# Optimization experiments

Hardware: AMD Instinct MI355X
Metric: run time of the kernel (lower is better)

## Reference

```python
import jax, jax.numpy as jnp
import numpy as np

B, O, GRID = 2048, 48, 112
SIGMA = 5.0


def setup_inputs() -> dict:
    key = jax.random.key(0)
    k1, k2, k3, k4, k5 = jax.random.split(key, 5)
    s = float(GRID - 1)
    xL = jax.random.uniform(k1, (B,), dtype=jnp.float32) * s
    yL = jax.random.uniform(k2, (B,), dtype=jnp.float32) * s
    obj_list = jax.random.uniform(k3, (B, O, 2), dtype=jnp.float32) * s
    obj_num = jax.random.randint(k4, (B,), 0, O + 1, dtype=jnp.int32)
    road_mask = jax.random.randint(k5, (B, GRID, GRID), 0, 2, dtype=jnp.int32)
    return {"xL": xL, "yL": yL, "obj_list": obj_list, "obj_num": obj_num,
            "road_mask": road_mask, "H": GRID, "W": GRID}


def reference(xL, yL, obj_list, obj_num, road_mask, H, W):
    # Faithful vectorization of batch_gaussian_tensor_obj.
    # exp(-(dx^2+dy^2)/(2s^2)) is separable: exp(-dx^2/..) * exp(-dy^2/..),
    # so per-object splats reduce to a batched matmul over the object axis.
    inv = 1.0 / (2.0 * SIGMA * SIGMA)
    x = jnp.arange(H, dtype=jnp.float32)  # row coordinate grid
    y = jnp.arange(W, dtype=jnp.float32)  # col coordinate grid

    # positive goal gaussian, rank-1 outer product per batch element
    gx = jnp.exp(-((x[None, :] - xL[:, None]) ** 2) * inv)  # [B,H]
    gy = jnp.exp(-((y[None, :] - yL[:, None]) ** 2) * inv)  # [B,W]
    goal = gx[:, :, None] * gy[:, None, :]                   # [B,H,W]

    # negative object gaussians; note original swaps xy: xo=xy[1], yo=xy[0]
    xo = obj_list[:, :, 1]  # [B,O] row coords
    yo = obj_list[:, :, 0]  # [B,O] col coords
    ex = jnp.exp(-((x[None, None, :] - xo[:, :, None]) ** 2) * inv)  # [B,O,H]
    ey = jnp.exp(-((y[None, None, :] - yo[:, :, None]) ** 2) * inv)  # [B,O,W]
    valid = (jnp.arange(O)[None, :] < obj_num[:, None]).astype(jnp.float32)  # [B,O]
    obj = jnp.einsum('boh,bow->bhw', ex * valid[:, :, None], ey)     # [B,H,W]

    channel = 0.5 + 0.5 * goal - 0.5 * obj
    channel = jnp.where(road_mask == 0, 0.0, channel)
    return channel
```

## Files before the change

### kernel.cpp

```cpp
#include <hip/hip_runtime.h>

#define GRID_N 112
#define O_MAX 48
#define HW_N (GRID_N * GRID_N)
#define NTHREADS 256

__global__ __launch_bounds__(NTHREADS) void goalmap_kernel(
    const float* __restrict__ xL, const float* __restrict__ yL,
    const float* __restrict__ obj_list, const int* __restrict__ obj_num,
    const int* __restrict__ road_mask, float* __restrict__ out)
{
    constexpr float INV = 1.0f / (2.0f * 5.0f * 5.0f);

    __shared__ float ex_s[O_MAX * GRID_N];
    __shared__ float ey_s[O_MAX * GRID_N];
    __shared__ float gx_s[GRID_N];
    __shared__ float gy_s[GRID_N];

    const int b   = blockIdx.x;
    const int tid = threadIdx.x;
    const int n   = obj_num[b];
    const float xl = xL[b];
    const float yl = yL[b];

    for (int i = tid; i < GRID_N; i += NTHREADS) {
        float dx = (float)i - xl;
        float dy = (float)i - yl;
        gx_s[i] = __expf(-dx * dx * INV);
        gy_s[i] = __expf(-dy * dy * INV);
    }
    for (int i = tid; i < n * GRID_N; i += NTHREADS) {
        int o = i / GRID_N;
        int p = i - o * GRID_N;
        float xo = obj_list[(b * O_MAX + o) * 2 + 1];
        float yo = obj_list[(b * O_MAX + o) * 2 + 0];
        float dx = (float)p - xo;
        float dy = (float)p - yo;
        ex_s[i] = __expf(-dx * dx * INV);
        ey_s[i] = __expf(-dy * dy * INV);
    }
    __syncthreads();

    const int*  rm = road_mask + (size_t)b * HW_N;
    float*      op = out       + (size_t)b * HW_N;

    const int NT = (GRID_N / 2) * (GRID_N / 4);
    for (int t = tid; t < NT; t += NTHREADS) {
        int hp = t / 28;
        int wq = t - hp * 28;
        int h = hp * 2;
        int w = wq * 4;

        float4 acc0 = make_float4(0.f, 0.f, 0.f, 0.f);
        float4 acc1 = make_float4(0.f, 0.f, 0.f, 0.f);

        #pragma unroll 4
        for (int o = 0; o < n; ++o) {
            float  ea = ex_s[o * GRID_N + h];
            float  eb = ex_s[o * GRID_N + h + 1];
            float4 ey = *(const float4*)&ey_s[o * GRID_N + w];
            acc0.x = fmaf(ea, ey.x, acc0.x);
            acc0.y = fmaf(ea, ey.y, acc0.y);
            acc0.z = fmaf(ea, ey.z, acc0.z);
            acc0.w = fmaf(ea, ey.w, acc0.w);
            acc1.x = fmaf(eb, ey.x, acc1.x);
            acc1.y = fmaf(eb, ey.y, acc1.y);
            acc1.z = fmaf(eb, ey.z, acc1.z);
            acc1.w = fmaf(eb, ey.w, acc1.w);
        }

        float  gxa = gx_s[h];
        float  gxb = gx_s[h + 1];
        float4 gy4 = *(const float4*)&gy_s[w];

        int base0 = h * GRID_N + w;
        int base1 = base0 + GRID_N;
        int4 m0 = *(const int4*)&rm[base0];
        int4 m1 = *(const int4*)&rm[base1];

        float4 v0, v1;
        v0.x = 0.5f + 0.5f * (gxa * gy4.x - acc0.x);
        v0.y = 0.5f + 0.5f * (gxa * gy4.y - acc0.y);
        v0.z = 0.5f + 0.5f * (gxa * gy4.z - acc0.z);
        v0.w = 0.5f + 0.5f * (gxa * gy4.w - acc0.w);
        v1.x = 0.5f + 0.5f * (gxb * gy4.x - acc1.x);
        v1.y = 0.5f + 0.5f * (gxb * gy4.y - acc1.y);
        v1.z = 0.5f + 0.5f * (gxb * gy4.z - acc1.z);
        v1.w = 0.5f + 0.5f * (gxb * gy4.w - acc1.w);

        v0.x = (m0.x == 0) ? 0.f : v0.x;
        v0.y = (m0.y == 0) ? 0.f : v0.y;
        v0.z = (m0.z == 0) ? 0.f : v0.z;
        v0.w = (m0.w == 0) ? 0.f : v0.w;
        v1.x = (m1.x == 0) ? 0.f : v1.x;
        v1.y = (m1.y == 0) ? 0.f : v1.y;
        v1.z = (m1.z == 0) ? 0.f : v1.z;
        v1.w = (m1.w == 0) ? 0.f : v1.w;

        *(float4*)&op[base0] = v0;
        *(float4*)&op[base1] = v1;
    }
}

extern "C" void kernel_launch(void* const* d_in, const int* in_sizes, int n_in,
                              void* d_out, int out_size, void* d_ws, size_t ws_size,
                              hipStream_t stream) {
    const float* xL       = (const float*)d_in[0];
    const float* yL       = (const float*)d_in[1];
    const float* obj_list = (const float*)d_in[2];
    const int*   obj_num  = (const int*)d_in[3];
    const int*   road_mask= (const int*)d_in[4];
    float*       out      = (float*)d_out;
    const int B = in_sizes[0];

    goalmap_kernel<<<B, NTHREADS, 0, stream>>>(xL, yL, obj_list, obj_num, road_mask, out);
}
```

Before: 214.4 us.

## Fold goal into object rank update, fp16 shared tables, 4x8 register tiles

Treats the goal Gaussian as one extra row of the rank-n outer product, with the 0.5 and sign scales folded into the shared table. The shared tables are stored in fp16 to halve LDS footprint and load bandwidth. Each thread now computes a 4x8 output tile instead of 2x4 to raise FMA-per-load reuse, and the block shrinks to 128 threads. Storing the tables in fp16 costs precision, and the larger per-thread tile increases register pressure.

```diff
diff --git a/kernel.cpp b/kernel.cpp
--- a/kernel.cpp
+++ b/kernel.cpp
@@ -3,115 +3,119 @@
 #define GRID_N 112
 #define O_MAX 48
 #define HW_N (GRID_N * GRID_N)
-#define NTHREADS 256
+#define NT 128
+#define ROWS_MAX (O_MAX + 1)
 
-__global__ __launch_bounds__(NTHREADS) void goalmap_kernel(
+typedef _Float16 half4_t __attribute__((ext_vector_type(4)));
+typedef _Float16 half8_t __attribute__((ext_vector_type(8)));
+
+__global__ __launch_bounds__(NT) void goalmap_kernel(
     const float* __restrict__ xL, const float* __restrict__ yL,
     const float* __restrict__ obj_list, const int* __restrict__ obj_num,
     const int* __restrict__ road_mask, float* __restrict__ out)
 {
     constexpr float INV = 1.0f / (2.0f * 5.0f * 5.0f);
 
-    __shared__ float ex_s[O_MAX * GRID_N];
-    __shared__ float ey_s[O_MAX * GRID_N];
-    __shared__ float gx_s[GRID_N];
-    __shared__ float gy_s[GRID_N];
+    __shared__ _Float16 sex[ROWS_MAX * GRID_N];
+    __shared__ _Float16 sey[ROWS_MAX * GRID_N];
 
     const int b   = blockIdx.x;
     const int tid = threadIdx.x;
     const int n   = obj_num[b];
+    const int rows = n + 1;
     const float xl = xL[b];
     const float yl = yL[b];
 
-    for (int i = tid; i < GRID_N; i += NTHREADS) {
-        float dx = (float)i - xl;
-        float dy = (float)i - yl;
-        gx_s[i] = __expf(-dx * dx * INV);
-        gy_s[i] = __expf(-dy * dy * INV);
-    }
-    for (int i = tid; i < n * GRID_N; i += NTHREADS) {
+    for (int i = tid; i < rows * GRID_N; i += NT) {
         int o = i / GRID_N;
         int p = i - o * GRID_N;
-        float xo = obj_list[(b * O_MAX + o) * 2 + 1];
-        float yo = obj_list[(b * O_MAX + o) * 2 + 0];
-        float dx = (float)p - xo;
-        float dy = (float)p - yo;
-        ex_s[i] = __expf(-dx * dx * INV);
-        ey_s[i] = __expf(-dy * dy * INV);
+        float cx, cy, sgn;
+        if (o < n) {
+            cx  = obj_list[(b * O_MAX + o) * 2 + 1];
+            cy  = obj_list[(b * O_MAX + o) * 2 + 0];
+            sgn = -0.5f;
+        } else {
+            cx  = xl;
+            cy  = yl;
+            sgn = 0.5f;
+        }
+        float dx = (float)p - cx;
+        float dy = (float)p - cy;
+        sex[i] = (_Float16)(sgn * __expf(-dx * dx * INV));
+        sey[i] = (_Float16)(__expf(-dy * dy * INV));
     }
     __syncthreads();
 
-    const int*  rm = road_mask + (size_t)b * HW_N;
-    float*      op = out       + (size_t)b * HW_N;
+    const int* rm = road_mask + (size_t)b * HW_N;
+    float*     op = out       + (size_t)b * HW_N;
 
-    const int NT = (GRID_N / 2) * (GRID_N / 4);
-    for (int t = tid; t < NT; t += NTHREADS) {
-        int hp = t / 28;
-        int wq = t - hp * 28;
-        int h = hp * 2;
-        int w = wq * 4;
+    const int NTILES = (GRID_N / 4) * (GRID_N / 8);
+    for (int t = tid; t < NTILES; t += NT) {
+        int hp = t / 14;
+        int wq = t - hp * 14;
+        int h = hp * 4;
+        int w = wq * 8;
 
-        float4 acc0 = make_float4(0.f, 0.f, 0.f, 0.f);
-        float4 acc1 = make_float4(0.f, 0.f, 0.f, 0.f);
+        float acc[4][8];
+        #pragma unroll
+        for (int r = 0; r < 4; ++r)
+            #pragma unroll
+            for (int c = 0; c < 8; ++c) acc[r][c] = 0.f;
 
-        #pragma unroll 4
-        for (int o = 0; o < n; ++o) {
-            float  ea = ex_s[o * GRID_N + h];
-            float  eb = ex_s[o * GRID_N + h + 1];
-            float4 ey = *(const float4*)&ey_s[o * GRID_N + w];
-            acc0.x = fmaf(ea, ey.x, acc0.x);
-            acc0.y = fmaf(ea, ey.y, acc0.y);
-            acc0.z = fmaf(ea, ey.z, acc0.z);
-            acc0.w = fmaf(ea, ey.w, acc0.w);
-            acc1.x = fmaf(eb, ey.x, acc1.x);
-            acc1.y = fmaf(eb, ey.y, acc1.y);
-            acc1.z = fmaf(eb, ey.z, acc1.z);
-            acc1.w = fmaf(eb, ey.w, acc1.w);
+        #pragma unroll 2
+        for (int o = 0; o < rows; ++o) {
+            half4_t ex4 = *(const half4_t*)&sex[o * GRID_N + h];
+            half8_t ey8 = *(const half8_t*)&sey[o * GRID_N + w];
+            float ef[4], gf[8];
+            #pragma unroll
+            for (int r = 0; r < 4; ++r) ef[r] = (float)ex4[r];
+            #pragma unroll
+            for (int c = 0; c < 8; ++c) gf[c] = (float)ey8[c];
+            #pragma unroll
+            for (int r = 0; r < 4; ++r)
+                #pragma unroll
+                for (int c = 0; c < 8; ++c)
+                    acc[r][c] = fmaf(ef[r], gf[c], acc[r][c]);
         }
 
-        float  gxa = gx_s[h];
-        float  gxb = gx_s[h + 1];
-        float4 gy4 = *(const float4*)&gy_s[w];
-
-        int base0 = h * GRID_N + w;
-        int base1 = base0 + GRID_N;
-        int4 m0 = *(const int4*)&rm[base0];
-        int4 m1 = *(const int4*)&rm[base1];
-
-        float4 v0, v1;
-        v0.x = 0.5f + 0.5f * (gxa * gy4.x - acc0.x);
-        v0.y = 0.5f + 0.5f * (gxa * gy4.y - acc0.y);
-        v0.z = 0.5f + 0.5f * (gxa * gy4.z - acc0.z);
-        v0.w = 0.5f + 0.5f * (gxa * gy4.w - acc0.w);
-        v1.x = 0.5f + 0.5f * (gxb * gy4.x - acc1.x);
-        v1.y = 0.5f + 0.5f * (gxb * gy4.y - acc1.y);
-        v1.z = 0.5f + 0.5f * (gxb * gy4.z - acc1.z);
-        v1.w = 0.5f + 0.5f * (gxb * gy4.w - acc1.w);
-
-        v0.x = (m0.x == 0) ? 0.f : v0.x;
-        v0.y = (m0.y == 0) ? 0.f : v0.y;
-        v0.z = (m0.z == 0) ? 0.f : v0.z;
-        v0.w = (m0.w == 0) ? 0.f : v0.w;
-        v1.x = (m1.x == 0) ? 0.f : v1.x;
-        v1.y = (m1.y == 0) ? 0.f : v1.y;
-        v1.z = (m1.z == 0) ? 0.f : v1.z;
-        v1.w = (m1.w == 0) ? 0.f : v1.w;
-
-        *(float4*)&op[base0] = v0;
-        *(float4*)&op[base1] = v1;
+        #pragma unroll
+        for (int r = 0; r < 4; ++r) {
+            int base = (h + r) * GRID_N + w;
+            int4 m0 = *(const int4*)&rm[base];
+            int4 m1 = *(const int4*)&rm[base + 4];
+            float4 v0, v1;
+            v0.x = 0.5f + acc[r][0];
+            v0.y = 0.5f + acc[r][1];
+            v0.z = 0.5f + acc[r][2];
+            v0.w = 0.5f + acc[r][3];
+            v1.x = 0.5f + acc[r][4];
+            v1.y = 0.5f + acc[r][5];
+            v1.z = 0.5f + acc[r][6];
+            v1.w = 0.5f + acc[r][7];
+            v0.x = (m0.x == 0) ? 0.f : v0.x;
+            v0.y = (m0.y == 0) ? 0.f : v0.y;
+            v0.z = (m0.z == 0) ? 0.f : v0.z;
+            v0.w = (m0.w == 0) ? 0.f : v0.w;
+            v1.x = (m1.x == 0) ? 0.f : v1.x;
+            v1.y = (m1.y == 0) ? 0.f : v1.y;
+            v1.z = (m1.z == 0) ? 0.f : v1.z;
+            v1.w = (m1.w == 0) ? 0.f : v1.w;
+            *(float4*)&op[base]     = v0;
+            *(float4*)&op[base + 4] = v1;
+        }
     }
 }
 
 extern "C" void kernel_launch(void* const* d_in, const int* in_sizes, int n_in,
                               void* d_out, int out_size, void* d_ws, size_t ws_size,
                               hipStream_t stream) {
-    const float* xL       = (const float*)d_in[0];
-    const float* yL       = (const float*)d_in[1];
-    const float* obj_list = (const float*)d_in[2];
-    const int*   obj_num  = (const int*)d_in[3];
-    const int*   road_mask= (const int*)d_in[4];
-    float*       out      = (float*)d_out;
+    const float* xL        = (const float*)d_in[0];
+    const float* yL        = (const float*)d_in[1];
+    const float* obj_list  = (const float*)d_in[2];
+    const int*   obj_num   = (const int*)d_in[3];
+    const int*   road_mask = (const int*)d_in[4];
+    float*       out       = (float*)d_out;
     const int B = in_sizes[0];
 
-    goalmap_kernel<<<B, NTHREADS, 0, stream>>>(xL, yL, obj_list, obj_num, road_mask, out);
+    goalmap_kernel<<<B, NT, 0, stream>>>(xL, yL, obj_list, obj_num, road_mask, out);
 }
```

New measurement: 222.0 us. 3.5% more time.
